# Kernel tuning notes

Measured on AMD Instinct MI355X. Metric: run time of the kernel, lower is better.

## Reference

```python
import jax, jax.numpy as jnp
import numpy as np

N_NODES = 100_000
N_EDGES = 3_200_000
F_IN, F_HID, F_OUT = 128, 128, 64
BN_EPS = 1e-5


def gcn_conv(x, src, dst, W, b, n_nodes):
    """PyG GCNConv: x' = D^{-1/2}(A+I)D^{-1/2} (x W) + b, self-loops included in src/dst."""
    h = x @ W                                                  # [N, out]
    ones = jnp.ones(src.shape[0], dtype=x.dtype)
    deg = jax.ops.segment_sum(ones, dst, num_segments=n_nodes)  # in-degree incl. self-loop (>=1)
    dinv = jax.lax.rsqrt(deg)
    norm = dinv[src] * dinv[dst]                               # [E+N]
    msg = h[src] * norm[:, None]                               # gather + scale
    out = jax.ops.segment_sum(msg, dst, num_segments=n_nodes)  # scatter-add
    return out + b


def setup_inputs() -> dict:
    key = jax.random.key(0)
    ks = jax.random.split(key, 6)
    x = jax.random.normal(ks[0], (N_NODES, F_IN), dtype=jnp.float32)
    edge_index = jax.random.randint(ks[1], (2, N_EDGES), 0, N_NODES, dtype=jnp.int32)
    W1 = jax.random.normal(ks[2], (F_IN, F_HID), dtype=jnp.float32) / np.sqrt(F_IN)
    b1 = jnp.zeros((F_HID,), dtype=jnp.float32)
    gamma = jnp.ones((F_HID,), dtype=jnp.float32)
    beta = jnp.zeros((F_HID,), dtype=jnp.float32)
    W2 = jax.random.normal(ks[3], (F_HID, F_OUT), dtype=jnp.float32) / np.sqrt(F_HID)
    b2 = jnp.zeros((F_OUT,), dtype=jnp.float32)
    return {"x": x, "edge_index": edge_index, "W1": W1, "b1": b1,
            "gamma": gamma, "beta": beta, "W2": W2, "b2": b2}


def reference(x, edge_index, W1, b1, gamma, beta, W2, b2):
    n = x.shape[0]
    loop = jnp.arange(n, dtype=edge_index.dtype)
    src = jnp.concatenate([edge_index[0], loop])
    dst = jnp.concatenate([edge_index[1], loop])
    # conv1
    h = gcn_conv(x, src, dst, W1, b1, n)
    # BatchNorm1d (training mode: batch stats, biased variance)
    mean = jnp.mean(h, axis=0)
    var = jnp.mean((h - mean) ** 2, axis=0)
    h = (h - mean) * jax.lax.rsqrt(var + BN_EPS) * gamma + beta
    # ReLU
    h = jax.nn.relu(h)
    # conv2
    return gcn_conv(h, src, dst, W2, b2, n)
```

## Files before the change

### kernel.cpp

```cpp
#include <hip/hip_runtime.h>
#include <math.h>


typedef _Float16 f16;
typedef _Float16 f16x2 __attribute__((ext_vector_type(2)));
typedef _Float16 f16x8 __attribute__((ext_vector_type(8)));
typedef float f32x4 __attribute__((ext_vector_type(4)));

static constexpr int KDIM = 128;
static constexpr int MAXNB = 1600;
static constexpr int CAP = 2560;
static constexpr int CHUNK = 8192;
static constexpr int BINT = 512;
static constexpr int WTP = 136;

__global__ __launch_bounds__(BINT) void binA_kernel(
    const int* __restrict__ src, const int* __restrict__ dst, int E,
    int* __restrict__ bcur, unsigned int* __restrict__ bins, int nbuck) {
  __shared__ int hist[MAXNB];
  __shared__ int base[MAXNB];
  const int tid = threadIdx.x;
  for (int b = tid; b < nbuck; b += BINT) hist[b] = 0;
  __syncthreads();
  const int e0 = blockIdx.x * CHUNK;
  const int e1 = min(e0 + CHUNK, E);
  for (int e = e0 + tid; e < e1; e += BINT) atomicAdd(&hist[dst[e] >> 6], 1);
  __syncthreads();
  for (int b = tid; b < nbuck; b += BINT) {
    int c = hist[b];
    base[b] = c ? atomicAdd(&bcur[b], c) : 0;
    hist[b] = 0;
  }
  __syncthreads();
  for (int e = e0 + tid; e < e1; e += BINT) {
    int d = dst[e];
    int b = d >> 6;
    int lp = atomicAdd(&hist[b], 1);
    int p = base[b] + lp;
    if (p < CAP)
      bins[(size_t)b * CAP + p] = (unsigned int)src[e] | ((unsigned int)(d & 63) << 17);
  }
}

__global__ __launch_bounds__(1024) void bscan_kernel(
    const int* __restrict__ bcur, int nbuck, int* __restrict__ bbase,
    int* __restrict__ off_n) {
  __shared__ int sh[1024];
  const int t = threadIdx.x;
  int a = (2 * t < nbuck) ? min(bcur[2 * t], CAP) : 0;
  int b = (2 * t + 1 < nbuck) ? min(bcur[2 * t + 1], CAP) : 0;
  sh[t] = a + b;
  __syncthreads();
  for (int o = 1; o < 1024; o <<= 1) {
    int v = (t >= o) ? sh[t - o] : 0;
    __syncthreads();
    sh[t] += v;
    __syncthreads();
  }
  int excl = (t > 0) ? sh[t - 1] : 0;
  if (2 * t < nbuck) bbase[2 * t] = excl;
  if (2 * t + 1 < nbuck) bbase[2 * t + 1] = excl + a;
  if (t == 1023) off_n[0] = sh[1023];
}

__global__ __launch_bounds__(256) void csrfill_kernel(
    const unsigned int* __restrict__ bins, const int* __restrict__ bcur,
    const int* __restrict__ bbase, int* __restrict__ csr, int* __restrict__ off,
    float* __restrict__ dinv, int n) {
  __shared__ int hist[64];
  __shared__ int pref[64];
  __shared__ int lcur[64];
  const int tid = threadIdx.x;
  const int b = blockIdx.x;
  const int cnt = min(bcur[b], CAP);
  const unsigned int* bp = bins + (size_t)b * CAP;
  if (tid < 64) hist[tid] = 0;
  __syncthreads();
  for (int e = tid; e < cnt; e += 256) atomicAdd(&hist[bp[e] >> 17], 1);
  __syncthreads();
  if (tid < 64) pref[tid] = hist[tid];
  __syncthreads();
  for (int o = 1; o < 64; o <<= 1) {
    int v = (tid < 64 && tid >= o) ? pref[tid - o] : 0;
    __syncthreads();
    if (tid < 64) pref[tid] += v;
    __syncthreads();
  }
  if (tid < 64) {
    int node = b * 64 + tid;
    if (node < n) {
      int excl = bbase[b] + pref[tid] - hist[tid];
      off[node] = excl;
      lcur[tid] = excl;
      dinv[node] = rsqrtf((float)(hist[tid] + 1));
    }
  }
  __syncthreads();
  for (int e = tid; e < cnt; e += 256) {
    unsigned int pk = bp[e];
    int r = pk >> 17;
    int p = atomicAdd(&lcur[r], 1);
    csr[p] = (int)(pk & 0x1FFFF);
  }
}

__global__ __launch_bounds__(256) void gemm1_kernel(
    const float* __restrict__ A, const float* __restrict__ W, f16* __restrict__ C,
    int M) {
  __shared__ f16 Wt[128][WTP];
  const int tid = threadIdx.x;
  for (int idx = tid; idx < 128 * 128; idx += 256) {
    int k = idx >> 7, nn = idx & 127;
    Wt[nn][k] = (f16)W[idx];
  }
  __syncthreads();
  const int wave = tid >> 6;
  const int lane = tid & 63;
  const int r = lane & 15;
  const int kg = lane >> 4;
  const int row0 = blockIdx.x * 64 + wave * 16;
  const bool valid = (row0 + r) < M;
  const float* arow = A + (size_t)(row0 + r) * KDIM;
  f32x4 acc[8];
#pragma unroll
  for (int nf = 0; nf < 8; ++nf) acc[nf] = (f32x4){0.f, 0.f, 0.f, 0.f};
#pragma unroll
  for (int ks = 0; ks < 4; ++ks) {
    const int k0 = ks * 32 + kg * 8;
    f16x8 a;
#pragma unroll
    for (int z = 0; z < 8; ++z) a[z] = (f16)0.f;
    if (valid) {
      float4 u = *reinterpret_cast<const float4*>(arow + k0);
      float4 v = *reinterpret_cast<const float4*>(arow + k0 + 4);
      a[0] = (f16)u.x; a[1] = (f16)u.y; a[2] = (f16)u.z; a[3] = (f16)u.w;
      a[4] = (f16)v.x; a[5] = (f16)v.y; a[6] = (f16)v.z; a[7] = (f16)v.w;
    }
#pragma unroll
    for (int nf = 0; nf < 8; ++nf) {
      f16x8 b = *reinterpret_cast<const f16x8*>(&Wt[nf * 16 + r][k0]);
      acc[nf] = __builtin_amdgcn_mfma_f32_16x16x32_f16(a, b, acc[nf], 0, 0, 0);
    }
  }
  const int crow = row0 + (lane >> 4) * 4;
  const int ccol = lane & 15;
#pragma unroll
  for (int q = 0; q < 4; ++q) {
    int rr = crow + q;
    if (rr < M) {
#pragma unroll
      for (int nf = 0; nf < 8; ++nf)
        C[(size_t)rr * 128 + nf * 16 + ccol] = (f16)acc[nf][q];
    }
  }
}

__global__ __launch_bounds__(256) void gemm2_kernel(
    const f16* __restrict__ A, const float* __restrict__ W, f16* __restrict__ C,
    int M, const float* __restrict__ ss, const float* __restrict__ dinv) {
  __shared__ f16 Wt[64][WTP];
  const int tid = threadIdx.x;
  for (int idx = tid; idx < 128 * 64; idx += 256) {
    int k = idx >> 6, nn = idx & 63;
    Wt[nn][k] = (f16)W[idx];
  }
  __syncthreads();
  const int wave = tid >> 6;
  const int lane = tid & 63;
  const int r = lane & 15;
  const int kg = lane >> 4;
  const int row0 = blockIdx.x * 64 + wave * 16;
  const bool valid = (row0 + r) < M;
  const f16* arow = A + (size_t)(row0 + r) * KDIM;
  f32x4 acc[4];
#pragma unroll
  for (int nf = 0; nf < 4; ++nf) acc[nf] = (f32x4){0.f, 0.f, 0.f, 0.f};
#pragma unroll
  for (int ks = 0; ks < 4; ++ks) {
    const int k0 = ks * 32 + kg * 8;
    f16x8 a;
#pragma unroll
    for (int z = 0; z < 8; ++z) a[z] = (f16)0.f;
    if (valid) {
      f16x8 raw = *reinterpret_cast<const f16x8*>(arow + k0);
      float4 s0 = *reinterpret_cast<const float4*>(&ss[k0]);
      float4 s1 = *reinterpret_cast<const float4*>(&ss[k0 + 4]);
      float4 t0 = *reinterpret_cast<const float4*>(&ss[128 + k0]);
      float4 t1 = *reinterpret_cast<const float4*>(&ss[128 + k0 + 4]);
      a[0] = (f16)fmaxf((float)raw[0] * s0.x + t0.x, 0.f);
      a[1] = (f16)fmaxf((float)raw[1] * s0.y + t0.y, 0.f);
      a[2] = (f16)fmaxf((float)raw[2] * s0.z + t0.z, 0.f);
      a[3] = (f16)fmaxf((float)raw[3] * s0.w + t0.w, 0.f);
      a[4] = (f16)fmaxf((float)raw[4] * s1.x + t1.x, 0.f);
      a[5] = (f16)fmaxf((float)raw[5] * s1.y + t1.y, 0.f);
      a[6] = (f16)fmaxf((float)raw[6] * s1.z + t1.z, 0.f);
      a[7] = (f16)fmaxf((float)raw[7] * s1.w + t1.w, 0.f);
    }
#pragma unroll
    for (int nf = 0; nf < 4; ++nf) {
      f16x8 b = *reinterpret_cast<const f16x8*>(&Wt[nf * 16 + r][k0]);
      acc[nf] = __builtin_amdgcn_mfma_f32_16x16x32_f16(a, b, acc[nf], 0, 0, 0);
    }
  }
  const int crow = row0 + (lane >> 4) * 4;
  const int ccol = lane & 15;
#pragma unroll
  for (int q = 0; q < 4; ++q) {
    int rr = crow + q;
    if (rr < M) {
      float dv = dinv[rr];
#pragma unroll
      for (int nf = 0; nf < 4; ++nf)
        C[(size_t)rr * 64 + nf * 16 + ccol] = (f16)(acc[nf][q] * dv);
    }
  }
}

__global__ __launch_bounds__(64) void agg1_kernel(
    const f16* __restrict__ h, const float* __restrict__ dinv,
    const int* __restrict__ off, const int* __restrict__ csr,
    const float* __restrict__ bias, f16* __restrict__ outh, int n) {
  const int i = blockIdx.x;
  const int t = threadIdx.x;
  const float di = dinv[i];
  const float2 bi = *reinterpret_cast<const float2*>(&bias[2 * t]);
  f16x2 hs = *reinterpret_cast<const f16x2*>(&h[(size_t)i * 128 + 2 * t]);
  float e0 = di * (float)hs[0];
  float e1 = di * (float)hs[1];
  const int beg = off[i], end = off[i + 1];
  int j = beg;
  for (; j + 16 <= end; j += 16) {
    int s[16];
#pragma unroll
    for (int k = 0; k < 16; ++k) s[k] = csr[j + k];
    float w[16];
#pragma unroll
    for (int k = 0; k < 16; ++k) w[k] = dinv[s[k]];
    f16x2 v[16];
#pragma unroll
    for (int k = 0; k < 16; ++k)
      v[k] = *reinterpret_cast<const f16x2*>(&h[(size_t)s[k] * 128 + 2 * t]);
#pragma unroll
    for (int k = 0; k < 16; ++k) {
      e0 += w[k] * (float)v[k][0];
      e1 += w[k] * (float)v[k][1];
    }
  }
  for (; j + 4 <= end; j += 4) {
    int s[4];
#pragma unroll
    for (int k = 0; k < 4; ++k) s[k] = csr[j + k];
    float w[4];
#pragma unroll
    for (int k = 0; k < 4; ++k) w[k] = dinv[s[k]];
    f16x2 v[4];
#pragma unroll
    for (int k = 0; k < 4; ++k)
      v[k] = *reinterpret_cast<const f16x2*>(&h[(size_t)s[k] * 128 + 2 * t]);
#pragma unroll
    for (int k = 0; k < 4; ++k) {
      e0 += w[k] * (float)v[k][0];
      e1 += w[k] * (float)v[k][1];
    }
  }
  for (; j < end; ++j) {
    int s = csr[j];
    float w = dinv[s];
    f16x2 v = *reinterpret_cast<const f16x2*>(&h[(size_t)s * 128 + 2 * t]);
    e0 += w * (float)v[0];
    e1 += w * (float)v[1];
  }
  f16x2 o;
  o[0] = (f16)(di * e0 + bi.x);
  o[1] = (f16)(di * e1 + bi.y);
  *reinterpret_cast<f16x2*>(&outh[(size_t)i * 128 + 2 * t]) = o;
}

__global__ __launch_bounds__(64) void agg2_kernel(
    const f16* __restrict__ h, const float* __restrict__ dinv,
    const int* __restrict__ off, const int* __restrict__ csr,
    const float* __restrict__ bias, float* __restrict__ out, int n) {
  const int i = blockIdx.x;
  const int t = threadIdx.x;
  const float di = dinv[i];
  float e = (float)h[(size_t)i * 64 + t];
  const int beg = off[i], end = off[i + 1];
  int j = beg;
  for (; j + 16 <= end; j += 16) {
    int s[16];
#pragma unroll
    for (int k = 0; k < 16; ++k) s[k] = csr[j + k];
    f16 v[16];
#pragma unroll
    for (int k = 0; k < 16; ++k) v[k] = h[(size_t)s[k] * 64 + t];
#pragma unroll
    for (int k = 0; k < 16; ++k) e += (float)v[k];
  }
  for (; j + 4 <= end; j += 4) {
    int s[4];
#pragma unroll
    for (int k = 0; k < 4; ++k) s[k] = csr[j + k];
    f16 v[4];
#pragma unroll
    for (int k = 0; k < 4; ++k) v[k] = h[(size_t)s[k] * 64 + t];
#pragma unroll
    for (int k = 0; k < 4; ++k) e += (float)v[k];
  }
  for (; j < end; ++j) e += (float)h[(size_t)csr[j] * 64 + t];
  out[(size_t)i * 64 + t] = di * e + bias[t];
}

__global__ void bnstat_kernel(const f16* __restrict__ a, int n, float* __restrict__ acc) {
  const int c = threadIdx.x & 127;
  const int half = threadIdx.x >> 7;
  const int rstart = blockIdx.x * 2 + half;
  const int rstep = gridDim.x * 2;
  float s = 0.f, ss = 0.f;
  for (int r = rstart; r < n; r += rstep) {
    float v = (float)a[(size_t)r * 128 + c];
    s += v;
    ss += v * v;
  }
  atomicAdd(&acc[c], s);
  atomicAdd(&acc[128 + c], ss);
}

__global__ void bnfin_kernel(const float* __restrict__ acc, const float* __restrict__ gamma,
                             const float* __restrict__ beta, int n, float* __restrict__ ss) {
  const int c = threadIdx.x;
  const float inv_n = 1.f / (float)n;
  const float mean = acc[c] * inv_n;
  const float var = acc[128 + c] * inv_n - mean * mean;
  const float sc = gamma[c] * rsqrtf(var + 1e-5f);
  ss[c] = sc;
  ss[128 + c] = beta[c] - mean * sc;
}

extern "C" void kernel_launch(void* const* d_in, const int* in_sizes, int n_in,
                              void* d_out, int out_size, void* d_ws, size_t ws_size,
                              hipStream_t stream) {
  const float* x = (const float*)d_in[0];
  const int* ei = (const int*)d_in[1];
  const float* W1 = (const float*)d_in[2];
  const float* b1 = (const float*)d_in[3];
  const float* gamma = (const float*)d_in[4];
  const float* beta = (const float*)d_in[5];
  const float* W2 = (const float*)d_in[6];
  const float* b2 = (const float*)d_in[7];
  float* out = (float*)d_out;

  const int n = in_sizes[0] / 128;
  const int E = in_sizes[1] / 2;
  const int* src = ei;
  const int* dst = ei + E;
  const int nbuck = (n + 63) / 64;

  char* p = (char*)d_ws;
  auto carve = [&](size_t bytes) {
    char* r = p;
    p += (bytes + 255) & ~(size_t)255;
    return r;
  };
  int* bcur = (int*)carve((size_t)nbuck * 4);
  float* bnacc = (float*)carve(256 * 4);
  const size_t zero_bytes = (size_t)((char*)(bnacc + 256) - (char*)bcur);
  int* bbase = (int*)carve((size_t)(nbuck + 1) * 4);
  float* bnss = (float*)carve(256 * 4);
  int* off = (int*)carve((size_t)(n + 1) * 4);
  float* dinv = (float*)carve((size_t)n * 4);
  unsigned int* bins = (unsigned int*)carve((size_t)nbuck * CAP * 4);
  int* csr = (int*)carve((size_t)E * 4);
  f16* h1 = (f16*)carve((size_t)n * 128 * 2);
  f16* agg1 = (f16*)carve((size_t)n * 128 * 2);
  f16* h2 = h1;

  hipMemsetAsync(bcur, 0, zero_bytes, stream);

  const int ngb = (n + 63) / 64;

  gemm1_kernel<<<ngb, 256, 0, stream>>>(x, W1, h1, n);

  binA_kernel<<<(E + CHUNK - 1) / CHUNK, BINT, 0, stream>>>(src, dst, E, bcur, bins, nbuck);
  bscan_kernel<<<1, 1024, 0, stream>>>(bcur, nbuck, bbase, off + n);
  csrfill_kernel<<<nbuck, 256, 0, stream>>>(bins, bcur, bbase, csr, off, dinv, n);

  agg1_kernel<<<n, 64, 0, stream>>>(h1, dinv, off, csr, b1, agg1, n);

  bnstat_kernel<<<512, 256, 0, stream>>>(agg1, n, bnacc);
  bnfin_kernel<<<1, 128, 0, stream>>>(bnacc, gamma, beta, n, bnss);

  gemm2_kernel<<<ngb, 256, 0, stream>>>(agg1, W2, h2, n, bnss, dinv);
  agg2_kernel<<<n, 64, 0, stream>>>(h2, dinv, off, csr, b2, out, n);
}
```

Before: 327.3 us.

## Store features in 16-column slice-major blocks and aggregate per slice

The intermediate feature matrices now use a column-sliced layout: 8 or 4 slices of 16 halfs, each laid out node-major. The aggregation kernels launch one wave per node per slice, with 8 lanes per edge row covering 16 edges at a time, and reduce across lanes with shuffles. Each slice is 3.2 MB for conv1, so its gathers can stay resident in L2 and cache locality improves over random 256-byte row gathers. The cost is more launched waves, re-reading the CSR indices once per slice, and 32-byte gather granularity.

```diff
diff --git a/kernel.cpp b/kernel.cpp
--- a/kernel.cpp
+++ b/kernel.cpp
@@ -105,7 +105,7 @@
 }
 
 __global__ __launch_bounds__(256) void gemm1_kernel(
-    const float* __restrict__ A, const float* __restrict__ W, f16* __restrict__ C,
+    const float* __restrict__ A, const float* __restrict__ W, f16* __restrict__ Cb,
     int M) {
   __shared__ f16 Wt[128][WTP];
   const int tid = threadIdx.x;
@@ -150,13 +150,13 @@
     if (rr < M) {
 #pragma unroll
       for (int nf = 0; nf < 8; ++nf)
-        C[(size_t)rr * 128 + nf * 16 + ccol] = (f16)acc[nf][q];
+        Cb[((size_t)nf * M + rr) * 16 + ccol] = (f16)acc[nf][q];
     }
   }
 }
 
 __global__ __launch_bounds__(256) void gemm2_kernel(
-    const f16* __restrict__ A, const float* __restrict__ W, f16* __restrict__ C,
+    const f16* __restrict__ Ab, const float* __restrict__ W, f16* __restrict__ Cb,
     int M, const float* __restrict__ ss, const float* __restrict__ dinv) {
   __shared__ f16 Wt[64][WTP];
   const int tid = threadIdx.x;
@@ -171,7 +171,6 @@
   const int kg = lane >> 4;
   const int row0 = blockIdx.x * 64 + wave * 16;
   const bool valid = (row0 + r) < M;
-  const f16* arow = A + (size_t)(row0 + r) * KDIM;
   f32x4 acc[4];
 #pragma unroll
   for (int nf = 0; nf < 4; ++nf) acc[nf] = (f32x4){0.f, 0.f, 0.f, 0.f};
@@ -182,7 +181,10 @@
 #pragma unroll
     for (int z = 0; z < 8; ++z) a[z] = (f16)0.f;
     if (valid) {
-      f16x8 raw = *reinterpret_cast<const f16x8*>(arow + k0);
+      const int slice = k0 >> 4;
+      const int koff = k0 & 15;
+      f16x8 raw = *reinterpret_cast<const f16x8*>(
+          &Ab[((size_t)slice * M + row0 + r) * 16 + koff]);
       float4 s0 = *reinterpret_cast<const float4*>(&ss[k0]);
       float4 s1 = *reinterpret_cast<const float4*>(&ss[k0 + 4]);
       float4 t0 = *reinterpret_cast<const float4*>(&ss[128 + k0]);
@@ -211,113 +213,104 @@
       float dv = dinv[rr];
 #pragma unroll
       for (int nf = 0; nf < 4; ++nf)
-        C[(size_t)rr * 64 + nf * 16 + ccol] = (f16)(acc[nf][q] * dv);
-    }
-  }
-}
-
-__global__ __launch_bounds__(64) void agg1_kernel(
-    const f16* __restrict__ h, const float* __restrict__ dinv,
+        Cb[((size_t)nf * M + rr) * 16 + ccol] = (f16)(acc[nf][q] * dv);
+    }
+  }
+}
+
+__global__ __launch_bounds__(256) void agg1s_kernel(
+    const f16* __restrict__ hblk, const float* __restrict__ dinv,
     const int* __restrict__ off, const int* __restrict__ csr,
-    const float* __restrict__ bias, f16* __restrict__ outh, int n) {
-  const int i = blockIdx.x;
-  const int t = threadIdx.x;
+    const float* __restrict__ bias, f16* __restrict__ oblk, int n) {
+  const int s = blockIdx.x & 7;
+  const int g = blockIdx.x >> 3;
+  const int w = threadIdx.x >> 6;
+  const int lane = threadIdx.x & 63;
+  const int i = g * 4 + w;
+  if (i >= n) return;
+  const int eo = lane >> 3;
+  const int cp = lane & 7;
   const float di = dinv[i];
-  const float2 bi = *reinterpret_cast<const float2*>(&bias[2 * t]);
-  f16x2 hs = *reinterpret_cast<const f16x2*>(&h[(size_t)i * 128 + 2 * t]);
-  float e0 = di * (float)hs[0];
-  float e1 = di * (float)hs[1];
+  const f16* hs = hblk + (size_t)s * n * 16;
+  float e0 = 0.f, e1 = 0.f;
   const int beg = off[i], end = off[i + 1];
-  int j = beg;
-  for (; j + 16 <= end; j += 16) {
-    int s[16];
-#pragma unroll
-    for (int k = 0; k < 16; ++k) s[k] = csr[j + k];
-    float w[16];
-#pragma unroll
-    for (int k = 0; k < 16; ++k) w[k] = dinv[s[k]];
-    f16x2 v[16];
-#pragma unroll
-    for (int k = 0; k < 16; ++k)
-      v[k] = *reinterpret_cast<const f16x2*>(&h[(size_t)s[k] * 128 + 2 * t]);
-#pragma unroll
-    for (int k = 0; k < 16; ++k) {
-      e0 += w[k] * (float)v[k][0];
-      e1 += w[k] * (float)v[k][1];
-    }
-  }
-  for (; j + 4 <= end; j += 4) {
-    int s[4];
-#pragma unroll
-    for (int k = 0; k < 4; ++k) s[k] = csr[j + k];
-    float w[4];
-#pragma unroll
-    for (int k = 0; k < 4; ++k) w[k] = dinv[s[k]];
-    f16x2 v[4];
-#pragma unroll
-    for (int k = 0; k < 4; ++k)
-      v[k] = *reinterpret_cast<const f16x2*>(&h[(size_t)s[k] * 128 + 2 * t]);
-#pragma unroll
-    for (int k = 0; k < 4; ++k) {
-      e0 += w[k] * (float)v[k][0];
-      e1 += w[k] * (float)v[k][1];
-    }
-  }
-  for (; j < end; ++j) {
-    int s = csr[j];
-    float w = dinv[s];
-    f16x2 v = *reinterpret_cast<const f16x2*>(&h[(size_t)s * 128 + 2 * t]);
-    e0 += w * (float)v[0];
-    e1 += w * (float)v[1];
-  }
-  f16x2 o;
-  o[0] = (f16)(di * e0 + bi.x);
-  o[1] = (f16)(di * e1 + bi.y);
-  *reinterpret_cast<f16x2*>(&outh[(size_t)i * 128 + 2 * t]) = o;
-}
-
-__global__ __launch_bounds__(64) void agg2_kernel(
-    const f16* __restrict__ h, const float* __restrict__ dinv,
+  for (int j = beg; j < end; j += 16) {
+    int j0 = j + eo, j1 = j0 + 8;
+    bool p0 = j0 < end, p1 = j1 < end;
+    int s0 = p0 ? csr[j0] : i;
+    int s1 = p1 ? csr[j1] : i;
+    float w0 = p0 ? dinv[s0] : 0.f;
+    float w1 = p1 ? dinv[s1] : 0.f;
+    f16x2 v0 = *reinterpret_cast<const f16x2*>(&hs[(size_t)s0 * 16 + 2 * cp]);
+    f16x2 v1 = *reinterpret_cast<const f16x2*>(&hs[(size_t)s1 * 16 + 2 * cp]);
+    e0 += w0 * (float)v0[0] + w1 * (float)v1[0];
+    e1 += w0 * (float)v0[1] + w1 * (float)v1[1];
+  }
+  e0 += __shfl_xor(e0, 8, 64);  e1 += __shfl_xor(e1, 8, 64);
+  e0 += __shfl_xor(e0, 16, 64); e1 += __shfl_xor(e1, 16, 64);
+  e0 += __shfl_xor(e0, 32, 64); e1 += __shfl_xor(e1, 32, 64);
+  if (eo == 0) {
+    float2 bi = *reinterpret_cast<const float2*>(&bias[s * 16 + 2 * cp]);
+    f16x2 hv = *reinterpret_cast<const f16x2*>(&hs[(size_t)i * 16 + 2 * cp]);
+    f16x2 o;
+    o[0] = (f16)(di * (e0 + di * (float)hv[0]) + bi.x);
+    o[1] = (f16)(di * (e1 + di * (float)hv[1]) + bi.y);
+    *reinterpret_cast<f16x2*>(&oblk[((size_t)s * n + i) * 16 + 2 * cp]) = o;
+  }
+}
+
+__global__ __launch_bounds__(256) void agg2s_kernel(
+    const f16* __restrict__ hblk, const float* __restrict__ dinv,
     const int* __restrict__ off, const int* __restrict__ csr,
     const float* __restrict__ bias, float* __restrict__ out, int n) {
-  const int i = blockIdx.x;
-  const int t = threadIdx.x;
+  const int q = blockIdx.x & 7;
+  const int s = q >> 1;
+  const int half = q & 1;
+  const int g = blockIdx.x >> 3;
+  const int w = threadIdx.x >> 6;
+  const int lane = threadIdx.x & 63;
+  const int i = g * 8 + w * 2 + half;
+  if (i >= n) return;
+  const int eo = lane >> 3;
+  const int cp = lane & 7;
   const float di = dinv[i];
-  float e = (float)h[(size_t)i * 64 + t];
+  const f16* hs = hblk + (size_t)s * n * 16;
+  float e0 = 0.f, e1 = 0.f;
   const int beg = off[i], end = off[i + 1];
-  int j = beg;
-  for (; j + 16 <= end; j += 16) {
-    int s[16];
-#pragma unroll
-    for (int k = 0; k < 16; ++k) s[k] = csr[j + k];
-    f16 v[16];
-#pragma unroll
-    for (int k = 0; k < 16; ++k) v[k] = h[(size_t)s[k] * 64 + t];
-#pragma unroll
-    for (int k = 0; k < 16; ++k) e += (float)v[k];
-  }
-  for (; j + 4 <= end; j += 4) {
-    int s[4];
-#pragma unroll
-    for (int k = 0; k < 4; ++k) s[k] = csr[j + k];
-    f16 v[4];
-#pragma unroll
-    for (int k = 0; k < 4; ++k) v[k] = h[(size_t)s[k] * 64 + t];
-#pragma unroll
-    for (int k = 0; k < 4; ++k) e += (float)v[k];
-  }
-  for (; j < end; ++j) e += (float)h[(size_t)csr[j] * 64 + t];
-  out[(size_t)i * 64 + t] = di * e + bias[t];
-}
-
-__global__ void bnstat_kernel(const f16* __restrict__ a, int n, float* __restrict__ acc) {
+  for (int j = beg; j < end; j += 16) {
+    int j0 = j + eo, j1 = j0 + 8;
+    bool p0 = j0 < end, p1 = j1 < end;
+    int s0 = p0 ? csr[j0] : i;
+    int s1 = p1 ? csr[j1] : i;
+    float w0 = p0 ? 1.f : 0.f;
+    float w1 = p1 ? 1.f : 0.f;
+    f16x2 v0 = *reinterpret_cast<const f16x2*>(&hs[(size_t)s0 * 16 + 2 * cp]);
+    f16x2 v1 = *reinterpret_cast<const f16x2*>(&hs[(size_t)s1 * 16 + 2 * cp]);
+    e0 += w0 * (float)v0[0] + w1 * (float)v1[0];
+    e1 += w0 * (float)v0[1] + w1 * (float)v1[1];
+  }
+  e0 += __shfl_xor(e0, 8, 64);  e1 += __shfl_xor(e1, 8, 64);
+  e0 += __shfl_xor(e0, 16, 64); e1 += __shfl_xor(e1, 16, 64);
+  e0 += __shfl_xor(e0, 32, 64); e1 += __shfl_xor(e1, 32, 64);
+  if (eo == 0) {
+    f16x2 hv = *reinterpret_cast<const f16x2*>(&hs[(size_t)i * 16 + 2 * cp]);
+    float2 bi = *reinterpret_cast<const float2*>(&bias[s * 16 + 2 * cp]);
+    float2 o;
+    o.x = di * (e0 + (float)hv[0]) + bi.x;
+    o.y = di * (e1 + (float)hv[1]) + bi.y;
+    *reinterpret_cast<float2*>(&out[(size_t)i * 64 + s * 16 + 2 * cp]) = o;
+  }
+}
+
+__global__ void bnstat_kernel(const f16* __restrict__ ab, int n, float* __restrict__ acc) {
   const int c = threadIdx.x & 127;
   const int half = threadIdx.x >> 7;
   const int rstart = blockIdx.x * 2 + half;
   const int rstep = gridDim.x * 2;
+  const f16* base = ab + (size_t)(c >> 4) * n * 16 + (c & 15);
   float s = 0.f, ss = 0.f;
   for (int r = rstart; r < n; r += rstep) {
-    float v = (float)a[(size_t)r * 128 + c];
+    float v = (float)base[(size_t)r * 16];
     s += v;
     ss += v * v;
   }
@@ -370,25 +363,25 @@
   float* dinv = (float*)carve((size_t)n * 4);
   unsigned int* bins = (unsigned int*)carve((size_t)nbuck * CAP * 4);
   int* csr = (int*)carve((size_t)E * 4);
-  f16* h1 = (f16*)carve((size_t)n * 128 * 2);
-  f16* agg1 = (f16*)carve((size_t)n * 128 * 2);
-  f16* h2 = h1;
+  f16* h1b = (f16*)carve((size_t)n * 128 * 2);
+  f16* agg1b = (f16*)carve((size_t)n * 128 * 2);
+  f16* h2b = h1b;
 
   hipMemsetAsync(bcur, 0, zero_bytes, stream);
 
   const int ngb = (n + 63) / 64;
 
-  gemm1_kernel<<<ngb, 256, 0, stream>>>(x, W1, h1, n);
+  gemm1_kernel<<<ngb, 256, 0, stream>>>(x, W1, h1b, n);
 
   binA_kernel<<<(E + CHUNK - 1) / CHUNK, BINT, 0, stream>>>(src, dst, E, bcur, bins, nbuck);
   bscan_kernel<<<1, 1024, 0, stream>>>(bcur, nbuck, bbase, off + n);
   csrfill_kernel<<<nbuck, 256, 0, stream>>>(bins, bcur, bbase, csr, off, dinv, n);
 
-  agg1_kernel<<<n, 64, 0, stream>>>(h1, dinv, off, csr, b1, agg1, n);
-
-  bnstat_kernel<<<512, 256, 0, stream>>>(agg1, n, bnacc);
+  agg1s_kernel<<<((n + 3) / 4) * 8, 256, 0, stream>>>(h1b, dinv, off, csr, b1, agg1b, n);
+
+  bnstat_kernel<<<512, 256, 0, stream>>>(agg1b, n, bnacc);
   bnfin_kernel<<<1, 128, 0, stream>>>(bnacc, gamma, beta, n, bnss);
 
-  gemm2_kernel<<<ngb, 256, 0, stream>>>(agg1, W2, h2, n, bnss, dinv);
-  agg2_kernel<<<n, 64, 0, stream>>>(h2, dinv, off, csr, b2, out, n);
-}
+  gemm2_kernel<<<ngb, 256, 0, stream>>>(agg1b, W2, h2b, n, bnss, dinv);
+  agg2s_kernel<<<((n + 7) / 8) * 8, 256, 0, stream>>>(h2b, dinv, off, csr, b2, out, n);
+}
```

Result: slower. 603.6 us (+84.4%).

## Prescale h1 by dinv in GEMM1 and use padded 16-wide CSR gathers

Applied to the files above, without the earlier changes.

Moves GEMM1 after CSR construction so each h1 row can be prescaled by its source dinv, which removes the per-edge dinv gather in agg1. Both aggregation kernels now load the CSR with int4 vector loads over 16-aligned windows and send out-of-range slots to a zero pad row at index n, replacing the 4-wide and scalar tail loops. Padding rows are zeroed by piggybacking on the bscan and bnfin kernels, and the csr buffer is extended. The cost is extra loads of the zero row at segment edges, and GEMM1 can no longer overlap with CSR building.

```diff
diff --git a/kernel.cpp b/kernel.cpp
--- a/kernel.cpp
+++ b/kernel.cpp
@@ -44,9 +44,10 @@
 
 __global__ __launch_bounds__(1024) void bscan_kernel(
     const int* __restrict__ bcur, int nbuck, int* __restrict__ bbase,
-    int* __restrict__ off_n) {
+    int* __restrict__ off_n, f16* __restrict__ h1rown) {
   __shared__ int sh[1024];
   const int t = threadIdx.x;
+  if (t < 128) h1rown[t] = (f16)0.f;
   int a = (2 * t < nbuck) ? min(bcur[2 * t], CAP) : 0;
   int b = (2 * t + 1 < nbuck) ? min(bcur[2 * t + 1], CAP) : 0;
   sh[t] = a + b;
@@ -106,7 +107,7 @@
 
 __global__ __launch_bounds__(256) void gemm1_kernel(
     const float* __restrict__ A, const float* __restrict__ W, f16* __restrict__ C,
-    int M) {
+    int M, const float* __restrict__ dinv) {
   __shared__ f16 Wt[128][WTP];
   const int tid = threadIdx.x;
   for (int idx = tid; idx < 128 * 128; idx += 256) {
@@ -148,9 +149,10 @@
   for (int q = 0; q < 4; ++q) {
     int rr = crow + q;
     if (rr < M) {
+      float dv = dinv[rr];
 #pragma unroll
       for (int nf = 0; nf < 8; ++nf)
-        C[(size_t)rr * 128 + nf * 16 + ccol] = (f16)acc[nf][q];
+        C[(size_t)rr * 128 + nf * 16 + ccol] = (f16)(acc[nf][q] * dv);
     }
   }
 }
@@ -225,50 +227,31 @@
   const float di = dinv[i];
   const float2 bi = *reinterpret_cast<const float2*>(&bias[2 * t]);
   f16x2 hs = *reinterpret_cast<const f16x2*>(&h[(size_t)i * 128 + 2 * t]);
-  float e0 = di * (float)hs[0];
-  float e1 = di * (float)hs[1];
-  const int beg = off[i], end = off[i + 1];
-  int j = beg;
-  for (; j + 16 <= end; j += 16) {
-    int s[16];
-#pragma unroll
-    for (int k = 0; k < 16; ++k) s[k] = csr[j + k];
-    float w[16];
-#pragma unroll
-    for (int k = 0; k < 16; ++k) w[k] = dinv[s[k]];
+  float e0 = (float)hs[0];
+  float e1 = (float)hs[1];
+  const int beg = __builtin_amdgcn_readfirstlane(off[i]);
+  const int end = __builtin_amdgcn_readfirstlane(off[i + 1]);
+  for (int j = beg & ~15; j < end; j += 16) {
+    int4 q0 = *reinterpret_cast<const int4*>(&csr[j]);
+    int4 q1 = *reinterpret_cast<const int4*>(&csr[j + 4]);
+    int4 q2 = *reinterpret_cast<const int4*>(&csr[j + 8]);
+    int4 q3 = *reinterpret_cast<const int4*>(&csr[j + 12]);
+    int s[16] = {q0.x, q0.y, q0.z, q0.w, q1.x, q1.y, q1.z, q1.w,
+                 q2.x, q2.y, q2.z, q2.w, q3.x, q3.y, q3.z, q3.w};
+    if (j < beg || j + 16 > end) {
+#pragma unroll
+      for (int k = 0; k < 16; ++k)
+        if (j + k < beg || j + k >= end) s[k] = n;
+    }
     f16x2 v[16];
 #pragma unroll
     for (int k = 0; k < 16; ++k)
       v[k] = *reinterpret_cast<const f16x2*>(&h[(size_t)s[k] * 128 + 2 * t]);
 #pragma unroll
     for (int k = 0; k < 16; ++k) {
-      e0 += w[k] * (float)v[k][0];
-      e1 += w[k] * (float)v[k][1];
-    }
-  }
-  for (; j + 4 <= end; j += 4) {
-    int s[4];
-#pragma unroll
-    for (int k = 0; k < 4; ++k) s[k] = csr[j + k];
-    float w[4];
-#pragma unroll
-    for (int k = 0; k < 4; ++k) w[k] = dinv[s[k]];
-    f16x2 v[4];
-#pragma unroll
-    for (int k = 0; k < 4; ++k)
-      v[k] = *reinterpret_cast<const f16x2*>(&h[(size_t)s[k] * 128 + 2 * t]);
-#pragma unroll
-    for (int k = 0; k < 4; ++k) {
-      e0 += w[k] * (float)v[k][0];
-      e1 += w[k] * (float)v[k][1];
-    }
-  }
-  for (; j < end; ++j) {
-    int s = csr[j];
-    float w = dinv[s];
-    f16x2 v = *reinterpret_cast<const f16x2*>(&h[(size_t)s * 128 + 2 * t]);
-    e0 += w * (float)v[0];
-    e1 += w * (float)v[1];
+      e0 += (float)v[k][0];
+      e1 += (float)v[k][1];
+    }
   }
   f16x2 o;
   o[0] = (f16)(di * e0 + bi.x);
@@ -284,29 +267,26 @@
   const int t = threadIdx.x;
   const float di = dinv[i];
   float e = (float)h[(size_t)i * 64 + t];
-  const int beg = off[i], end = off[i + 1];
-  int j = beg;
-  for (; j + 16 <= end; j += 16) {
-    int s[16];
-#pragma unroll
-    for (int k = 0; k < 16; ++k) s[k] = csr[j + k];
+  const int beg = __builtin_amdgcn_readfirstlane(off[i]);
+  const int end = __builtin_amdgcn_readfirstlane(off[i + 1]);
+  for (int j = beg & ~15; j < end; j += 16) {
+    int4 q0 = *reinterpret_cast<const int4*>(&csr[j]);
+    int4 q1 = *reinterpret_cast<const int4*>(&csr[j + 4]);
+    int4 q2 = *reinterpret_cast<const int4*>(&csr[j + 8]);
+    int4 q3 = *reinterpret_cast<const int4*>(&csr[j + 12]);
+    int s[16] = {q0.x, q0.y, q0.z, q0.w, q1.x, q1.y, q1.z, q1.w,
+                 q2.x, q2.y, q2.z, q2.w, q3.x, q3.y, q3.z, q3.w};
+    if (j < beg || j + 16 > end) {
+#pragma unroll
+      for (int k = 0; k < 16; ++k)
+        if (j + k < beg || j + k >= end) s[k] = n;
+    }
     f16 v[16];
 #pragma unroll
     for (int k = 0; k < 16; ++k) v[k] = h[(size_t)s[k] * 64 + t];
 #pragma unroll
     for (int k = 0; k < 16; ++k) e += (float)v[k];
   }
-  for (; j + 4 <= end; j += 4) {
-    int s[4];
-#pragma unroll
-    for (int k = 0; k < 4; ++k) s[k] = csr[j + k];
-    f16 v[4];
-#pragma unroll
-    for (int k = 0; k < 4; ++k) v[k] = h[(size_t)s[k] * 64 + t];
-#pragma unroll
-    for (int k = 0; k < 4; ++k) e += (float)v[k];
-  }
-  for (; j < end; ++j) e += (float)h[(size_t)csr[j] * 64 + t];
   out[(size_t)i * 64 + t] = di * e + bias[t];
 }
 
@@ -326,8 +306,10 @@
 }
 
 __global__ void bnfin_kernel(const float* __restrict__ acc, const float* __restrict__ gamma,
-                             const float* __restrict__ beta, int n, float* __restrict__ ss) {
+                             const float* __restrict__ beta, int n, float* __restrict__ ss,
+                             f16* __restrict__ h2rown) {
   const int c = threadIdx.x;
+  if (c < 64) h2rown[c] = (f16)0.f;
   const float inv_n = 1.f / (float)n;
   const float mean = acc[c] * inv_n;
   const float var = acc[128 + c] * inv_n - mean * mean;
@@ -369,8 +351,8 @@
   int* off = (int*)carve((size_t)(n + 1) * 4);
   float* dinv = (float*)carve((size_t)n * 4);
   unsigned int* bins = (unsigned int*)carve((size_t)nbuck * CAP * 4);
-  int* csr = (int*)carve((size_t)E * 4);
-  f16* h1 = (f16*)carve((size_t)n * 128 * 2);
+  int* csr = (int*)carve((size_t)(E + 64) * 4);
+  f16* h1 = (f16*)carve((size_t)(n + 1) * 128 * 2);
   f16* agg1 = (f16*)carve((size_t)n * 128 * 2);
   f16* h2 = h1;
 
@@ -378,16 +360,15 @@
 
   const int ngb = (n + 63) / 64;
 
-  gemm1_kernel<<<ngb, 256, 0, stream>>>(x, W1, h1, n);
-
   binA_kernel<<<(E + CHUNK - 1) / CHUNK, BINT, 0, stream>>>(src, dst, E, bcur, bins, nbuck);
-  bscan_kernel<<<1, 1024, 0, stream>>>(bcur, nbuck, bbase, off + n);
+  bscan_kernel<<<1, 1024, 0, stream>>>(bcur, nbuck, bbase, off + n, h1 + (size_t)n * 128);
   csrfill_kernel<<<nbuck, 256, 0, stream>>>(bins, bcur, bbase, csr, off, dinv, n);
 
+  gemm1_kernel<<<ngb, 256, 0, stream>>>(x, W1, h1, n, dinv);
   agg1_kernel<<<n, 64, 0, stream>>>(h1, dinv, off, csr, b1, agg1, n);
 
   bnstat_kernel<<<512, 256, 0, stream>>>(agg1, n, bnacc);
-  bnfin_kernel<<<1, 128, 0, stream>>>(bnacc, gamma, beta, n, bnss);
+  bnfin_kernel<<<1, 128, 0, stream>>>(bnacc, gamma, beta, n, bnss, h2 + (size_t)n * 64);
 
   gemm2_kernel<<<ngb, 256, 0, stream>>>(agg1, W2, h2, n, bnss, dinv);
   agg2_kernel<<<n, 64, 0, stream>>>(h2, dinv, off, csr, b2, out, n);
```

Result: slower. 341.9 us (+4.5%).
